# Performance work log

Hardware: AMD Instinct MI355X
Metric: run time of the kernel (lower is better)

Reference implementation:

```python
import jax, jax.numpy as jnp
import numpy as np

S = 4096      # sequence length == contextlen
D_IN = 1024   # input_size
E = 512       # embed_dim = input_size // 2 (divisor=2)
OUT = 256     # output_size (action dim)
HEAD_DIM = 2  # E // num_heads, num_heads = input_size // 4 = 256


def _w(k, shape):
    return jax.random.normal(k, shape, dtype=jnp.float32) * 0.02


def setup_inputs() -> dict:
    key = jax.random.key(0)
    ks = jax.random.split(key, 12)
    return {
        "x": jax.random.normal(ks[0], (S, D_IN), dtype=jnp.float32),
        # Encoder: D_IN -> 2D -> 4D -> 2D -> E (torch Linear: y = x W^T + b)
        "enc_w1": _w(ks[1], (2 * D_IN, D_IN)), "enc_b1": jnp.zeros((2 * D_IN,), jnp.float32),
        "enc_w2": _w(ks[2], (4 * D_IN, 2 * D_IN)), "enc_b2": jnp.zeros((4 * D_IN,), jnp.float32),
        "enc_w3": _w(ks[3], (2 * D_IN, 4 * D_IN)), "enc_b3": jnp.zeros((2 * D_IN,), jnp.float32),
        "enc_w4": _w(ks[4], (E, 2 * D_IN)), "enc_b4": jnp.zeros((E,), jnp.float32),
        # MultiheadDiffAttention packed qkv + out projection + lambda
        "in_proj_w": _w(ks[5], (3 * E, E)), "in_proj_b": jnp.zeros((3 * E,), jnp.float32),
        "out_proj_w": _w(ks[6], (E, E)), "out_proj_b": jnp.zeros((E,), jnp.float32),
        "lam": jnp.float32(0.8),
        # Actor head: E -> D_IN -> 2D_IN -> OUT
        "act_w1": _w(ks[7], (D_IN, E)), "act_b1": jnp.zeros((D_IN,), jnp.float32),
        "act_w2": _w(ks[8], (2 * D_IN, D_IN)), "act_b2": jnp.zeros((2 * D_IN,), jnp.float32),
        "act_w3": _w(ks[9], (OUT, 2 * D_IN)), "act_b3": jnp.zeros((OUT,), jnp.float32),
    }


def _pos_encoding(seq_len, d):
    pos = jnp.arange(seq_len, dtype=jnp.float32)[:, None]
    div = jnp.exp(jnp.arange(0, d, 2, dtype=jnp.float32) * (-np.log(10000.0) / d))
    pe = jnp.zeros((seq_len, d), jnp.float32)
    pe = pe.at[:, 0::2].set(jnp.sin(pos * div))
    pe = pe.at[:, 1::2].set(jnp.cos(pos * div))
    return pe


def reference(x, enc_w1, enc_b1, enc_w2, enc_b2, enc_w3, enc_b3, enc_w4, enc_b4,
              in_proj_w, in_proj_b, out_proj_w, out_proj_b, lam,
              act_w1, act_b1, act_w2, act_b2, act_w3, act_b3):
    relu = jax.nn.relu
    # Encoder MLP
    h = relu(x @ enc_w1.T + enc_b1)
    h = relu(h @ enc_w2.T + enc_b2)
    h = relu(h @ enc_w3.T + enc_b3)
    h = h @ enc_w4.T + enc_b4                      # (S, E)
    # Positional add
    h = h + _pos_encoding(S, E)
    # Differential dual-softmax attention (unbatched, heads never split)
    qkv = h @ in_proj_w.T + in_proj_b              # (S, 3E)
    q, k, v = jnp.split(qkv, 3, axis=-1)
    q1, q2 = jnp.split(q, 2, axis=-1)              # (S, E/2) each
    k1, k2 = jnp.split(k, 2, axis=-1)
    scale = 1.0 / np.sqrt(HEAD_DIM)
    a1 = jax.nn.softmax(jnp.matmul(q1, k1.T) * scale, axis=-1)   # (S, S)
    a2 = jax.nn.softmax(jnp.matmul(q2, k2.T) * scale, axis=-1)   # (S, S)
    # faithful quirk: boolean triu mask is ADDED (as 0/1) post-softmax
    causal_add = jnp.triu(jnp.ones((S, S), jnp.float32), k=1)
    diff = a1 - lam * a2 + causal_add
    attn_out = jnp.matmul(diff, v)                 # (S, E)
    # faithful quirk: transpose(0,1) then row-major view(S, -1, E)
    attn_out = jnp.reshape(attn_out.T, (S, 1, E))
    attn_out = attn_out @ out_proj_w.T + out_proj_b
    h = attn_out[:, 0, :]                          # squeeze(1)
    # Actor head
    h = relu(h @ act_w1.T + act_b1)
    h = relu(h @ act_w2.T + act_b2)
    h = h @ act_w3.T + act_b3                      # (S, OUT)
    logits = h[-1]                                 # (OUT,)
    return jax.nn.softmax(logits, axis=0)
```

## Files before the change

### kernel.cpp

```cpp
#include <hip/hip_runtime.h>
#include <cstdint>
#include <cstddef>

typedef __bf16 bf16x8 __attribute__((ext_vector_type(8)));
typedef float  f32x4  __attribute__((ext_vector_type(4)));

#define LDS_AS __attribute__((address_space(3)))
#define GLB_AS __attribute__((address_space(1)))

static __device__ __forceinline__ unsigned short f2bf(float f) {
    unsigned int u = __float_as_uint(f);
    u += 0x7fffu + ((u >> 16) & 1u);
    return (unsigned short)(u >> 16);
}

__global__ __launch_bounds__(256) void cvt_f32_bf16(const float* __restrict__ in,
                                                    unsigned short* __restrict__ out, int n4) {
    int stride = gridDim.x * blockDim.x;
    for (int i = blockIdx.x * blockDim.x + threadIdx.x; i < n4; i += stride) {
        float4 f = reinterpret_cast<const float4*>(in)[i];
        ushort4 u;
        u.x = f2bf(f.x); u.y = f2bf(f.y); u.z = f2bf(f.z); u.w = f2bf(f.w);
        reinterpret_cast<ushort4*>(out)[i] = u;
    }
}

__global__ void divtab_kernel(float* __restrict__ dtab) {
    int i = threadIdx.x;
    dtab[i] = expf((float)(2 * i) * (-9.210340371976184f / 512.0f));
}

template<int EPI>
__global__ __launch_bounds__(256) void gemm_bt(
    const unsigned short* __restrict__ A, int lda,
    const unsigned short* __restrict__ B, int ldb,
    int M, int N, int K,
    const float* __restrict__ bias,
    unsigned short* __restrict__ Cb, float* __restrict__ Cf, int ldc,
    float scale, const float* __restrict__ dtab)
{
    __shared__ unsigned short ldsA[128 * 32];
    __shared__ unsigned short ldsB[128 * 32];

    const int nbn = N >> 7;
    const int bm = blockIdx.x / nbn, bn = blockIdx.x % nbn;
    const int t = threadIdx.x;
    const int lane = t & 63, wid = t >> 6;
    const int wr = wid >> 1, wc = wid & 1;
    const int l15 = lane & 15, l4 = lane >> 4;

    const unsigned short* ga0 = A + (size_t)(bm * 128 + (t >> 2)) * lda + (t & 3) * 8;
    const unsigned short* gb0 = B + (size_t)(bn * 128 + (t >> 2)) * ldb + (t & 3) * 8;
    const size_t a64 = (size_t)64 * lda, b64 = (size_t)64 * ldb;
    LDS_AS void* laD0 = (LDS_AS void*)(&ldsA[wid * 512]);
    LDS_AS void* laD1 = (LDS_AS void*)(&ldsA[2048 + wid * 512]);
    LDS_AS void* lbD0 = (LDS_AS void*)(&ldsB[wid * 512]);
    LDS_AS void* lbD1 = (LDS_AS void*)(&ldsB[2048 + wid * 512]);

    const bf16x8* pa = (const bf16x8*)&ldsA[(wr * 64 + l15) * 32 + l4 * 8];
    const bf16x8* pb = (const bf16x8*)&ldsB[(wc * 64 + l15) * 32 + l4 * 8];

    f32x4 acc[4][4];
    const f32x4 z = {0.f, 0.f, 0.f, 0.f};
#pragma unroll
    for (int i = 0; i < 4; i++)
#pragma unroll
        for (int j = 0; j < 4; j++) acc[i][j] = z;

    const int nk = K >> 5;
    for (int kt = 0; kt < nk; ++kt) {
        const unsigned short* ga = ga0 + kt * 32;
        const unsigned short* gb = gb0 + kt * 32;
        __builtin_amdgcn_global_load_lds((const GLB_AS void*)ga,         laD0, 16, 0, 0);
        __builtin_amdgcn_global_load_lds((const GLB_AS void*)(ga + a64), laD1, 16, 0, 0);
        __builtin_amdgcn_global_load_lds((const GLB_AS void*)gb,         lbD0, 16, 0, 0);
        __builtin_amdgcn_global_load_lds((const GLB_AS void*)(gb + b64), lbD1, 16, 0, 0);
        __syncthreads();

        bf16x8 af[4], bfr[4];
#pragma unroll
        for (int mi = 0; mi < 4; mi++) af[mi]  = pa[mi * 64];
#pragma unroll
        for (int ni = 0; ni < 4; ni++) bfr[ni] = pb[ni * 64];
#pragma unroll
        for (int mi = 0; mi < 4; mi++)
#pragma unroll
            for (int ni = 0; ni < 4; ni++)
                acc[mi][ni] = __builtin_amdgcn_mfma_f32_16x16x32_bf16(af[mi], bfr[ni], acc[mi][ni], 0, 0, 0);
        __syncthreads();
    }

    const int row0 = bm * 128 + wr * 64;
    const int col0 = bn * 128 + wc * 64;
#pragma unroll
    for (int mi = 0; mi < 4; mi++) {
#pragma unroll
        for (int ni = 0; ni < 4; ni++) {
            f32x4 c = acc[mi][ni];
            const int col = col0 + ni * 16 + l15;
            float bv = 0.f, dv = 0.f;
            if (EPI != 3) bv = bias[col];
            if (EPI == 2) dv = dtab[col >> 1];
#pragma unroll
            for (int r = 0; r < 4; r++) {
                const int row = row0 + mi * 16 + l4 * 4 + r;
                float v = c[r] + bv;
                if (EPI == 0) v = fmaxf(v, 0.f);
                if (EPI == 2) {
                    float ang = (float)row * dv;
                    v += (col & 1) ? cosf(ang) : sinf(ang);
                }
                if (EPI == 3) {
                    Cf[(size_t)row * ldc + col] = v * scale;
                } else {
                    Cb[(size_t)row * ldc + col] = f2bf(v);
                    if (EPI == 2) Cf[(size_t)row * ldc + col] = v;
                }
            }
        }
    }
}

__global__ __launch_bounds__(256) void vcol_kernel(const float* __restrict__ Hf,
                                                   const float* __restrict__ ipw,
                                                   const float* __restrict__ ipb,
                                                   float* __restrict__ v) {
    const int row = blockIdx.x * 4 + (threadIdx.x >> 6);
    const int lane = threadIdx.x & 63;
    const float* w = ipw + (size_t)1535 * 512;
    const float* h = Hf + (size_t)row * 512;
    float s = 0.f;
    for (int k = lane; k < 512; k += 64) s += h[k] * w[k];
#pragma unroll
    for (int off = 32; off; off >>= 1) s += __shfl_down(s, off);
    if (lane == 0) v[row] = s + ipb[1535];
}

__global__ __launch_bounds__(256) void attn_rows(const float* __restrict__ S1,
                                                 const float* __restrict__ S2,
                                                 const float* __restrict__ v,
                                                 const float* __restrict__ lamp,
                                                 float* __restrict__ out) {
    const int r = blockIdx.x;
    const int tid = threadIdx.x, lane = tid & 63, wid = tid >> 6;
    const float* s1 = S1 + (size_t)r * 4096;
    const float* s2 = S2 + (size_t)r * 4096;
    __shared__ float red[4][8];

    float m1 = -1e30f, m2 = -1e30f;
    for (int i = tid; i < 4096; i += 256) {
        m1 = fmaxf(m1, s1[i]);
        m2 = fmaxf(m2, s2[i]);
    }
#pragma unroll
    for (int off = 32; off; off >>= 1) {
        m1 = fmaxf(m1, __shfl_down(m1, off));
        m2 = fmaxf(m2, __shfl_down(m2, off));
    }
    if (lane == 0) { red[wid][0] = m1; red[wid][1] = m2; }
    __syncthreads();
    m1 = fmaxf(fmaxf(red[0][0], red[1][0]), fmaxf(red[2][0], red[3][0]));
    m2 = fmaxf(fmaxf(red[0][1], red[1][1]), fmaxf(red[2][1], red[3][1]));

    const int gj = 3584 + r;
    float e1 = 0.f, e2 = 0.f, d1 = 0.f, d2 = 0.f, cs = 0.f;
    for (int i = tid; i < 4096; i += 256) {
        float p1 = expf(s1[i] - m1);
        float p2 = expf(s2[i] - m2);
        float vv = v[i];
        e1 += p1; e2 += p2; d1 += p1 * vv; d2 += p2 * vv;
        if (i > gj) cs += vv;
    }
#pragma unroll
    for (int off = 32; off; off >>= 1) {
        e1 += __shfl_down(e1, off); e2 += __shfl_down(e2, off);
        d1 += __shfl_down(d1, off); d2 += __shfl_down(d2, off);
        cs += __shfl_down(cs, off);
    }
    __syncthreads();
    if (lane == 0) {
        red[wid][0] = e1; red[wid][1] = e2; red[wid][2] = d1; red[wid][3] = d2; red[wid][4] = cs;
    }
    __syncthreads();
    if (tid == 0) {
        e1 = red[0][0] + red[1][0] + red[2][0] + red[3][0];
        e2 = red[0][1] + red[1][1] + red[2][1] + red[3][1];
        d1 = red[0][2] + red[1][2] + red[2][2] + red[3][2];
        d2 = red[0][3] + red[1][3] + red[2][3] + red[3][3];
        cs = red[0][4] + red[1][4] + red[2][4] + red[3][4];
        out[r] = d1 / e1 - lamp[0] * (d2 / e2) + cs;
    }
}

template<int RELU>
__global__ __launch_bounds__(256) void matvec(const float* __restrict__ W, const float* __restrict__ x,
                                              const float* __restrict__ b, float* __restrict__ y,
                                              int N, int K) {
    const int o = blockIdx.x * 4 + (threadIdx.x >> 6);
    const int lane = threadIdx.x & 63;
    if (o >= N) return;
    const float* w = W + (size_t)o * K;
    float s = 0.f;
    for (int k = lane; k < K; k += 64) s += w[k] * x[k];
#pragma unroll
    for (int off = 32; off; off >>= 1) s += __shfl_down(s, off);
    if (lane == 0) y[o] = RELU ? fmaxf(s + b[o], 0.f) : (s + b[o]);
}

__global__ __launch_bounds__(256) void softmax256(const float* __restrict__ lg, float* __restrict__ out) {
    const int tid = threadIdx.x, lane = tid & 63, wid = tid >> 6;
    __shared__ float rm[4], rs[4];
    float l = lg[tid];
    float m = l;
#pragma unroll
    for (int off = 32; off; off >>= 1) m = fmaxf(m, __shfl_down(m, off));
    if (lane == 0) rm[wid] = m;
    __syncthreads();
    m = fmaxf(fmaxf(rm[0], rm[1]), fmaxf(rm[2], rm[3]));
    float e = expf(l - m);
    float s = e;
#pragma unroll
    for (int off = 32; off; off >>= 1) s += __shfl_down(s, off);
    if (lane == 0) rs[wid] = s;
    __syncthreads();
    s = rs[0] + rs[1] + rs[2] + rs[3];
    out[tid] = e / s;
}

extern "C" void kernel_launch(void* const* d_in, const int* in_sizes, int n_in,
                              void* d_out, int out_size, void* d_ws, size_t ws_size,
                              hipStream_t stream) {
    const float* x      = (const float*)d_in[0];
    const float* enc_w1 = (const float*)d_in[1];
    const float* enc_b1 = (const float*)d_in[2];
    const float* enc_w2 = (const float*)d_in[3];
    const float* enc_b2 = (const float*)d_in[4];
    const float* enc_w3 = (const float*)d_in[5];
    const float* enc_b3 = (const float*)d_in[6];
    const float* enc_w4 = (const float*)d_in[7];
    const float* enc_b4 = (const float*)d_in[8];
    const float* ipw    = (const float*)d_in[9];
    const float* ipb    = (const float*)d_in[10];
    const float* opw    = (const float*)d_in[11];
    const float* opb    = (const float*)d_in[12];
    const float* lam    = (const float*)d_in[13];
    const float* aw1    = (const float*)d_in[14];
    const float* ab1    = (const float*)d_in[15];
    const float* aw2    = (const float*)d_in[16];
    const float* ab2    = (const float*)d_in[17];
    const float* aw3    = (const float*)d_in[18];
    const float* ab3    = (const float*)d_in[19];

    char* ws = (char*)d_ws;
    const size_t MB = 1ull << 20;
    unsigned short* bufA = (unsigned short*)(ws);
    unsigned short* bufB = (unsigned short*)(ws + 32 * MB);
    float* S1            = (float*)(ws + 32 * MB);
    float* S2            = (float*)(ws + 40 * MB);
    unsigned short* Wb   = (unsigned short*)(ws + 48 * MB);
    unsigned short* IPb  = (unsigned short*)(ws + 64 * MB);
    unsigned short* Hb   = (unsigned short*)(ws + 66 * MB);
    float* Hf            = (float*)(ws + 70 * MB);
    unsigned short* Kb   = (unsigned short*)(ws + 78 * MB);
    unsigned short* Qb   = (unsigned short*)(ws + 82 * MB);
    float* vcol          = (float*)(ws + 83 * MB);
    float* dtab          = (float*)(ws + 83 * MB + 64 * 1024);
    float* attnv         = (float*)(ws + 83 * MB + 128 * 1024);
    float* hh            = (float*)(ws + 83 * MB + 192 * 1024);
    float* h1            = (float*)(ws + 83 * MB + 256 * 1024);
    float* h2            = (float*)(ws + 83 * MB + 320 * 1024);
    float* lg            = (float*)(ws + 83 * MB + 384 * 1024);

    auto cvt = [&](const float* in, unsigned short* outp, int n) {
        int n4 = n >> 2;
        int blocks = (n4 + 255) / 256;
        if (blocks > 2048) blocks = 2048;
        cvt_f32_bf16<<<dim3(blocks), dim3(256), 0, stream>>>(in, outp, n4);
    };

    divtab_kernel<<<dim3(1), dim3(256), 0, stream>>>(dtab);

    cvt(x, bufA, 4096 * 1024);
    cvt(enc_w1, Wb, 2048 * 1024);
    gemm_bt<0><<<dim3(32 * 16), dim3(256), 0, stream>>>(bufA, 1024, Wb, 1024, 4096, 2048, 1024,
                                                        enc_b1, bufB, nullptr, 2048, 1.f, nullptr);
    cvt(enc_w2, Wb, 4096 * 2048);
    gemm_bt<0><<<dim3(32 * 32), dim3(256), 0, stream>>>(bufB, 2048, Wb, 2048, 4096, 4096, 2048,
                                                        enc_b2, bufA, nullptr, 4096, 1.f, nullptr);
    cvt(enc_w3, Wb, 2048 * 4096);
    gemm_bt<0><<<dim3(32 * 16), dim3(256), 0, stream>>>(bufA, 4096, Wb, 4096, 4096, 2048, 4096,
                                                        enc_b3, bufB, nullptr, 2048, 1.f, nullptr);
    cvt(enc_w4, Wb, 512 * 2048);
    gemm_bt<2><<<dim3(32 * 4), dim3(256), 0, stream>>>(bufB, 2048, Wb, 2048, 4096, 512, 2048,
                                                       enc_b4, Hb, Hf, 512, 1.f, dtab);

    cvt(ipw, IPb, 1536 * 512);
    gemm_bt<1><<<dim3(32 * 4), dim3(256), 0, stream>>>(Hb, 512, IPb + 512 * 512, 512, 4096, 512, 512,
                                                       ipb + 512, Kb, nullptr, 512, 1.f, nullptr);
    gemm_bt<1><<<dim3(4 * 4), dim3(256), 0, stream>>>(Hb + (size_t)3584 * 512, 512, IPb, 512, 512, 512, 512,
                                                      ipb, Qb, nullptr, 512, 1.f, nullptr);
    vcol_kernel<<<dim3(1024), dim3(256), 0, stream>>>(Hf, ipw, ipb, vcol);

    const float rs2 = 0.70710678118654752f;
    gemm_bt<3><<<dim3(4 * 32), dim3(256), 0, stream>>>(Qb, 512, Kb, 512, 512, 4096, 256,
                                                       nullptr, nullptr, S1, 4096, rs2, nullptr);
    gemm_bt<3><<<dim3(4 * 32), dim3(256), 0, stream>>>(Qb + 256, 512, Kb + 256, 512, 512, 4096, 256,
                                                       nullptr, nullptr, S2, 4096, rs2, nullptr);

    attn_rows<<<dim3(512), dim3(256), 0, stream>>>(S1, S2, vcol, lam, attnv);

    matvec<0><<<dim3(128), dim3(256), 0, stream>>>(opw, attnv, opb, hh, 512, 512);
    matvec<1><<<dim3(256), dim3(256), 0, stream>>>(aw1, hh, ab1, h1, 1024, 512);
    matvec<1><<<dim3(512), dim3(256), 0, stream>>>(aw2, h1, ab2, h2, 2048, 1024);
    matvec<0><<<dim3(64), dim3(256), 0, stream>>>(aw3, h2, ab3, lg, 256, 2048);
    softmax256<<<dim3(1), dim3(256), 0, stream>>>(lg, (float*)d_out);
}
```

Baseline: 680.6 us.

## Add 256x256-tile pipelined GEMM kernel for the three large encoder layers

Introduces a new 512-thread GEMM with 256x256 output tiles, a 4-deep LDS ring filled through direct global-to-LDS loads issued two k-steps ahead, XOR-swizzled LDS layout, and an XCD-aware block remap. The first three encoder GEMMs switch to it to raise arithmetic intensity per tile and overlap global loads with MFMA work. In exchange the kernel holds 128 accumulator vectors per thread and uses 128 KB of LDS, and its grids (128 or 256 blocks) are small relative to the CU count, so wave-quantisation and occupancy could limit gains.

```diff
diff --git a/kernel.cpp b/kernel.cpp
--- a/kernel.cpp
+++ b/kernel.cpp
@@ -28,6 +28,134 @@
 __global__ void divtab_kernel(float* __restrict__ dtab) {
     int i = threadIdx.x;
     dtab[i] = expf((float)(2 * i) * (-9.210340371976184f / 512.0f));
+}
+
+template<int EPI>
+__global__ __launch_bounds__(512, 2) void gemm256_bt(
+    const unsigned short* __restrict__ A, int lda,
+    const unsigned short* __restrict__ B, int ldb,
+    int M, int N, int K,
+    const float* __restrict__ bias,
+    unsigned short* __restrict__ Cb, int ldc)
+{
+    __shared__ __align__(16) unsigned short lds[4][2][8192];
+
+    const int nbn = N >> 8;
+    int wg = blockIdx.x;
+    {
+        int q = gridDim.x >> 3;
+        wg = (wg & 7) * q + (wg >> 3);
+    }
+    const int bm = wg / nbn, bn = wg % nbn;
+
+    const int t = threadIdx.x;
+    const int lane = t & 63, wid = t >> 6;
+    const int wr = wid >> 2, wc = wid & 3;
+    const int l15 = lane & 15, l4 = lane >> 4;
+
+    const int sr = t >> 2;
+    const int ss = (t & 3) ^ ((sr >> 1) & 3);
+    const unsigned short* gA0 = A + (size_t)(bm * 256 + sr      ) * lda + ss * 8;
+    const unsigned short* gA1 = A + (size_t)(bm * 256 + sr + 128) * lda + ss * 8;
+    const unsigned short* gB0 = B + (size_t)(bn * 256 + sr      ) * ldb + ss * 8;
+    const unsigned short* gB1 = B + (size_t)(bn * 256 + sr + 128) * ldb + ss * 8;
+
+    const int rsw  = ((l4 ^ ((l15 >> 1) & 3)) << 4);
+    const int aoff = (wr * 128 + l15) * 64 + rsw;
+    const int boff = (wc * 64  + l15) * 64 + rsw;
+
+    f32x4 acc[8][4];
+    const f32x4 z = {0.f, 0.f, 0.f, 0.f};
+#pragma unroll
+    for (int i = 0; i < 8; i++)
+#pragma unroll
+        for (int j = 0; j < 4; j++) acc[i][j] = z;
+
+    const int nk = K >> 5;
+
+#define STAGE_A(kt_) do { int b_ = (kt_) & 3;                                              \
+        __builtin_amdgcn_global_load_lds((const GLB_AS void*)(gA0 + (kt_) * 32),           \
+            (LDS_AS void*)&lds[b_][0][wid * 512], 16, 0, 0);                               \
+        __builtin_amdgcn_global_load_lds((const GLB_AS void*)(gA1 + (kt_) * 32),           \
+            (LDS_AS void*)&lds[b_][0][4096 + wid * 512], 16, 0, 0); } while (0)
+#define STAGE_B(kt_) do { int b_ = (kt_) & 3;                                              \
+        __builtin_amdgcn_global_load_lds((const GLB_AS void*)(gB0 + (kt_) * 32),           \
+            (LDS_AS void*)&lds[b_][1][wid * 512], 16, 0, 0);                               \
+        __builtin_amdgcn_global_load_lds((const GLB_AS void*)(gB1 + (kt_) * 32),           \
+            (LDS_AS void*)&lds[b_][1][4096 + wid * 512], 16, 0, 0); } while (0)
+
+    STAGE_A(0); STAGE_B(0);
+    STAGE_A(1); STAGE_B(1);
+    asm volatile("s_waitcnt vmcnt(4)" ::: "memory");
+    __builtin_amdgcn_s_barrier();
+    __builtin_amdgcn_sched_barrier(0);
+
+    for (int kt = 0; kt < nk; ++kt) {
+        const int b = kt & 3;
+        const LDS_AS char* abase = (const LDS_AS char*)&lds[b][0][0] + aoff;
+        const LDS_AS char* bbase = (const LDS_AS char*)&lds[b][1][0] + boff;
+
+        bf16x8 af[4], bfr[4];
+#pragma unroll
+        for (int i = 0; i < 4; ++i) af[i]  = *(const LDS_AS bf16x8*)(abase + i * 1024);
+#pragma unroll
+        for (int j = 0; j < 4; ++j) bfr[j] = *(const LDS_AS bf16x8*)(bbase + j * 1024);
+        if (kt + 2 < nk) STAGE_A(kt + 2);
+        __builtin_amdgcn_s_barrier();
+        asm volatile("s_waitcnt lgkmcnt(0)" ::: "memory");
+        __builtin_amdgcn_sched_barrier(0);
+        __builtin_amdgcn_s_setprio(1);
+#pragma unroll
+        for (int i = 0; i < 4; ++i)
+#pragma unroll
+            for (int j = 0; j < 4; ++j)
+                acc[i][j] = __builtin_amdgcn_mfma_f32_16x16x32_bf16(af[i], bfr[j], acc[i][j], 0, 0, 0);
+        __builtin_amdgcn_s_setprio(0);
+        __builtin_amdgcn_sched_barrier(0);
+        __builtin_amdgcn_s_barrier();
+
+#pragma unroll
+        for (int i = 0; i < 4; ++i) af[i] = *(const LDS_AS bf16x8*)(abase + 4096 + i * 1024);
+        if (kt + 2 < nk) {
+            STAGE_B(kt + 2);
+            asm volatile("s_waitcnt vmcnt(4)" ::: "memory");
+        } else {
+            asm volatile("s_waitcnt vmcnt(0)" ::: "memory");
+        }
+        __builtin_amdgcn_s_barrier();
+        asm volatile("s_waitcnt lgkmcnt(0)" ::: "memory");
+        __builtin_amdgcn_sched_barrier(0);
+        __builtin_amdgcn_s_setprio(1);
+#pragma unroll
+        for (int i = 0; i < 4; ++i)
+#pragma unroll
+            for (int j = 0; j < 4; ++j)
+                acc[4 + i][j] = __builtin_amdgcn_mfma_f32_16x16x32_bf16(af[i], bfr[j], acc[4 + i][j], 0, 0, 0);
+        __builtin_amdgcn_s_setprio(0);
+        __builtin_amdgcn_sched_barrier(0);
+        __builtin_amdgcn_s_barrier();
+    }
+#undef STAGE_A
+#undef STAGE_B
+
+    const int row0 = bm * 256 + wr * 128;
+    const int col0 = bn * 256 + wc * 64;
+#pragma unroll
+    for (int mi = 0; mi < 8; mi++) {
+#pragma unroll
+        for (int ni = 0; ni < 4; ni++) {
+            f32x4 c = acc[mi][ni];
+            const int col = col0 + ni * 16 + l15;
+            const float bv = bias[col];
+#pragma unroll
+            for (int r = 0; r < 4; r++) {
+                const int row = row0 + mi * 16 + l4 * 4 + r;
+                float v = c[r] + bv;
+                if (EPI == 0) v = fmaxf(v, 0.f);
+                Cb[(size_t)row * ldc + col] = f2bf(v);
+            }
+        }
+    }
 }
 
 template<int EPI>
@@ -282,14 +410,14 @@
 
     cvt(x, bufA, 4096 * 1024);
     cvt(enc_w1, Wb, 2048 * 1024);
-    gemm_bt<0><<<dim3(32 * 16), dim3(256), 0, stream>>>(bufA, 1024, Wb, 1024, 4096, 2048, 1024,
-                                                        enc_b1, bufB, nullptr, 2048, 1.f, nullptr);
+    gemm256_bt<0><<<dim3(16 * 8), dim3(512), 0, stream>>>(bufA, 1024, Wb, 1024, 4096, 2048, 1024,
+                                                          enc_b1, bufB, 2048);
     cvt(enc_w2, Wb, 4096 * 2048);
-    gemm_bt<0><<<dim3(32 * 32), dim3(256), 0, stream>>>(bufB, 2048, Wb, 2048, 4096, 4096, 2048,
-                                                        enc_b2, bufA, nullptr, 4096, 1.f, nullptr);
+    gemm256_bt<0><<<dim3(16 * 16), dim3(512), 0, stream>>>(bufB, 2048, Wb, 2048, 4096, 4096, 2048,
+                                                           enc_b2, bufA, 4096);
     cvt(enc_w3, Wb, 2048 * 4096);
-    gemm_bt<0><<<dim3(32 * 16), dim3(256), 0, stream>>>(bufA, 4096, Wb, 4096, 4096, 2048, 4096,
-                                                        enc_b3, bufB, nullptr, 2048, 1.f, nullptr);
+    gemm256_bt<0><<<dim3(16 * 8), dim3(512), 0, stream>>>(bufA, 4096, Wb, 4096, 4096, 2048, 4096,
+                                                          enc_b3, bufB, 2048);
     cvt(enc_w4, Wb, 512 * 2048);
     gemm_bt<2><<<dim3(32 * 4), dim3(256), 0, stream>>>(bufB, 2048, Wb, 2048, 4096, 512, 2048,
                                                        enc_b4, Hb, Hf, 512, 1.f, dtab);
```

After: 655.1 us. 3.8% less time.

## Add triple-buffered 128x256 MFMA GEMM with direct-to-LDS loads for encoder layers

Applied to the files above, without the earlier changes.

Introduces a new 512-thread GEMM kernel with 128x256 tiles, K=64 steps, triple-buffered LDS staging via global_load_lds, XOR-swizzled layout, and an XCD-aware block remap. It replaces the first three encoder GEMMs, which dominate the FLOPs. The goal is to hide global memory latency behind MFMA work, raise data reuse per tile, and reduce LDS bank conflicts. In exchange it uses a large LDS footprint that limits occupancy, relies on fine-grained barriers and waitcnt tuning, and produces fewer workgroups for the smaller layers.

```diff
diff --git a/kernel.cpp b/kernel.cpp
--- a/kernel.cpp
+++ b/kernel.cpp
@@ -1,6 +1,7 @@
 #include <hip/hip_runtime.h>
 #include <cstdint>
 #include <cstddef>
+
 
 typedef __bf16 bf16x8 __attribute__((ext_vector_type(8)));
 typedef float  f32x4  __attribute__((ext_vector_type(4)));
@@ -28,6 +29,137 @@
 __global__ void divtab_kernel(float* __restrict__ dtab) {
     int i = threadIdx.x;
     dtab[i] = expf((float)(2 * i) * (-9.210340371976184f / 512.0f));
+}
+
+template<int ID>
+__global__ __launch_bounds__(512, 2) void gemm8p(
+    const unsigned short* __restrict__ A, int lda,
+    const unsigned short* __restrict__ B, int ldb,
+    int M, int N, int K,
+    const float* __restrict__ bias,
+    unsigned short* __restrict__ Cb, int ldc)
+{
+    constexpr int ABYTES = 128 * 64 * 2;
+    constexpr int SLOT   = ABYTES + 256 * 64 * 2;
+    __shared__ __align__(16) unsigned char lds[3 * SLOT];
+
+    const int nbn = N >> 8;
+    int wg = blockIdx.x;
+    { int q = gridDim.x >> 3; wg = (wg & 7) * q + (wg >> 3); }
+    const int bm = wg / nbn, bn = wg % nbn;
+
+    const int t = threadIdx.x;
+    const int lane = t & 63, wid = t >> 6;
+    const int wr = wid >> 2, wc = wid & 3;
+    const int l15 = lane & 15, l4 = lane >> 4;
+
+    const int srow = t >> 3, sj = t & 7;
+    const int skA = (sj ^ (srow & 7)) * 8;
+    const unsigned short* gA = A + (size_t)(bm * 128 + srow) * lda + skA;
+    const unsigned short* gB = B + (size_t)(bn * 256 + srow) * ldb + skA;
+    const size_t a64 = (size_t)64 * lda, b64 = (size_t)64 * ldb;
+
+    const int ks0 = ((0 * 4 + l4) ^ (l15 & 7)) * 16;
+    const int ks1 = ((1 * 4 + l4) ^ (l15 & 7)) * 16;
+    const int arow = (wr * 64 + l15) * 128;
+    const int brow = ABYTES + (wc * 64 + l15) * 128;
+
+    f32x4 acc[4][4];
+    const f32x4 z = {0.f, 0.f, 0.f, 0.f};
+#pragma unroll
+    for (int i = 0; i < 4; i++)
+#pragma unroll
+        for (int j = 0; j < 4; j++) acc[i][j] = z;
+
+    const int nt = K >> 6;
+
+#define STAGE(kt_) do { unsigned char* d_ = &lds[((kt_) % 3) * SLOT];                       \
+        const unsigned short* a_ = gA + (size_t)(kt_) * 64;                                 \
+        const unsigned short* b_ = gB + (size_t)(kt_) * 64;                                 \
+        __builtin_amdgcn_global_load_lds((const GLB_AS void*)a_,         (LDS_AS void*)(d_ + t * 16),                 16, 0, 0); \
+        __builtin_amdgcn_global_load_lds((const GLB_AS void*)(a_ + a64), (LDS_AS void*)(d_ + 8192 + t * 16),          16, 0, 0); \
+        __builtin_amdgcn_global_load_lds((const GLB_AS void*)b_,         (LDS_AS void*)(d_ + ABYTES + t * 16),        16, 0, 0); \
+        __builtin_amdgcn_global_load_lds((const GLB_AS void*)(b_ + b64), (LDS_AS void*)(d_ + ABYTES + 8192 + t * 16), 16, 0, 0); \
+        __builtin_amdgcn_global_load_lds((const GLB_AS void*)(b_ + 2 * b64), (LDS_AS void*)(d_ + ABYTES + 16384 + t * 16), 16, 0, 0); \
+        __builtin_amdgcn_global_load_lds((const GLB_AS void*)(b_ + 3 * b64), (LDS_AS void*)(d_ + ABYTES + 24576 + t * 16), 16, 0, 0); \
+    } while (0)
+
+    STAGE(0);
+    STAGE(1);
+    asm volatile("s_waitcnt vmcnt(6)" ::: "memory");
+    __builtin_amdgcn_s_barrier();
+    __builtin_amdgcn_sched_barrier(0);
+
+    for (int kt = 0; kt < nt; ++kt) {
+        const LDS_AS unsigned char* s = (const LDS_AS unsigned char*)&lds[(kt % 3) * SLOT];
+
+        bf16x8 af[4][2], bf[2][2];
+#pragma unroll
+        for (int mi = 0; mi < 4; ++mi) {
+            af[mi][0] = *(const LDS_AS bf16x8*)(s + arow + mi * 2048 + ks0);
+            af[mi][1] = *(const LDS_AS bf16x8*)(s + arow + mi * 2048 + ks1);
+        }
+#pragma unroll
+        for (int ni = 0; ni < 2; ++ni) {
+            bf[ni][0] = *(const LDS_AS bf16x8*)(s + brow + ni * 2048 + ks0);
+            bf[ni][1] = *(const LDS_AS bf16x8*)(s + brow + ni * 2048 + ks1);
+        }
+        if (kt + 2 < nt) STAGE(kt + 2);
+        __builtin_amdgcn_s_barrier();
+        asm volatile("s_waitcnt lgkmcnt(0)" ::: "memory");
+        __builtin_amdgcn_sched_barrier(0);
+        __builtin_amdgcn_s_setprio(1);
+#pragma unroll
+        for (int mi = 0; mi < 4; ++mi)
+#pragma unroll
+            for (int ni = 0; ni < 2; ++ni) {
+                acc[mi][ni] = __builtin_amdgcn_mfma_f32_16x16x32_bf16(af[mi][0], bf[ni][0], acc[mi][ni], 0, 0, 0);
+                acc[mi][ni] = __builtin_amdgcn_mfma_f32_16x16x32_bf16(af[mi][1], bf[ni][1], acc[mi][ni], 0, 0, 0);
+            }
+        __builtin_amdgcn_s_setprio(0);
+        __builtin_amdgcn_sched_barrier(0);
+        __builtin_amdgcn_s_barrier();
+
+#pragma unroll
+        for (int ni = 0; ni < 2; ++ni) {
+            bf[ni][0] = *(const LDS_AS bf16x8*)(s + brow + (2 + ni) * 2048 + ks0);
+            bf[ni][1] = *(const LDS_AS bf16x8*)(s + brow + (2 + ni) * 2048 + ks1);
+        }
+        if (kt + 2 < nt) asm volatile("s_waitcnt vmcnt(6)" ::: "memory");
+        else             asm volatile("s_waitcnt vmcnt(0)" ::: "memory");
+        __builtin_amdgcn_s_barrier();
+        asm volatile("s_waitcnt lgkmcnt(0)" ::: "memory");
+        __builtin_amdgcn_sched_barrier(0);
+        __builtin_amdgcn_s_setprio(1);
+#pragma unroll
+        for (int mi = 0; mi < 4; ++mi)
+#pragma unroll
+            for (int ni = 0; ni < 2; ++ni) {
+                acc[mi][2 + ni] = __builtin_amdgcn_mfma_f32_16x16x32_bf16(af[mi][0], bf[ni][0], acc[mi][2 + ni], 0, 0, 0);
+                acc[mi][2 + ni] = __builtin_amdgcn_mfma_f32_16x16x32_bf16(af[mi][1], bf[ni][1], acc[mi][2 + ni], 0, 0, 0);
+            }
+        __builtin_amdgcn_s_setprio(0);
+        __builtin_amdgcn_sched_barrier(0);
+        __builtin_amdgcn_s_barrier();
+    }
+#undef STAGE
+
+    const int row0 = bm * 128 + wr * 64;
+    const int col0 = bn * 256 + wc * 64;
+#pragma unroll
+    for (int mi = 0; mi < 4; mi++) {
+#pragma unroll
+        for (int ni = 0; ni < 4; ni++) {
+            f32x4 c = acc[mi][ni];
+            const int col = col0 + ni * 16 + l15;
+            const float bv = bias[col];
+#pragma unroll
+            for (int r = 0; r < 4; r++) {
+                const int row = row0 + mi * 16 + l4 * 4 + r;
+                Cb[(size_t)row * ldc + col] = f2bf(fmaxf(c[r] + bv, 0.f));
+            }
+        }
+    }
 }
 
 template<int EPI>
@@ -282,14 +414,14 @@
 
     cvt(x, bufA, 4096 * 1024);
     cvt(enc_w1, Wb, 2048 * 1024);
-    gemm_bt<0><<<dim3(32 * 16), dim3(256), 0, stream>>>(bufA, 1024, Wb, 1024, 4096, 2048, 1024,
-                                                        enc_b1, bufB, nullptr, 2048, 1.f, nullptr);
+    gemm8p<1><<<dim3(32 * 8), dim3(512), 0, stream>>>(bufA, 1024, Wb, 1024,
+                                                      4096, 2048, 1024, enc_b1, bufB, 2048);
     cvt(enc_w2, Wb, 4096 * 2048);
-    gemm_bt<0><<<dim3(32 * 32), dim3(256), 0, stream>>>(bufB, 2048, Wb, 2048, 4096, 4096, 2048,
-                                                        enc_b2, bufA, nullptr, 4096, 1.f, nullptr);
+    gemm8p<2><<<dim3(32 * 16), dim3(512), 0, stream>>>(bufB, 2048, Wb, 2048,
+                                                       4096, 4096, 2048, enc_b2, bufA, 4096);
     cvt(enc_w3, Wb, 2048 * 4096);
-    gemm_bt<0><<<dim3(32 * 16), dim3(256), 0, stream>>>(bufA, 4096, Wb, 4096, 4096, 2048, 4096,
-                                                        enc_b3, bufB, nullptr, 2048, 1.f, nullptr);
+    gemm8p<3><<<dim3(32 * 8), dim3(512), 0, stream>>>(bufA, 4096, Wb, 4096,
+                                                      4096, 2048, 4096, enc_b3, bufB, 2048);
     cvt(enc_w4, Wb, 512 * 2048);
     gemm_bt<2><<<dim3(32 * 4), dim3(256), 0, stream>>>(bufB, 2048, Wb, 2048, 4096, 512, 2048,
                                                        enc_b4, Hb, Hf, 512, 1.f, dtab);
```

After: 621.9 us. 8.6% less time.
